# Performance work log

Measured on AMD Instinct MI355X. Metric: run time of the kernel, lower is better.

The kernel has to match this reference:

```python
import jax, jax.numpy as jnp
import numpy as np

T, B, E, H, V, L = 128, 64, 1024, 1024, 10000, 2  # emb_size must equal hidden_size (see decode layer)


def setup_inputs() -> dict:
    key = jax.random.key(0)
    ks = jax.random.split(key, 8)
    s = 0.05
    return {
        "inputs": jax.random.randint(ks[0], (T, B), 0, V),
        "hidden": jnp.zeros((L, B, H), jnp.float32),
        "emb_table": jax.random.normal(ks[1], (V, E), jnp.float32) * s,
        "Ww": jax.random.normal(ks[2], (L, H, E), jnp.float32) * s,
        "Wb": jnp.zeros((L, H), jnp.float32),
        "Uw": jax.random.normal(ks[3], (L, H, H), jnp.float32) * s,
        "Ub": jnp.zeros((L, H), jnp.float32),
        "Fw": jax.random.normal(ks[4], (L, E, H), jnp.float32) * s,
        "Fb": jnp.zeros((L, E), jnp.float32),
        "Dw": jax.random.normal(ks[5], (V, H), jnp.float32) * s,
        "Db": jnp.zeros((V,), jnp.float32),
    }


def reference(inputs, hidden, emb_table, Ww, Wb, Uw, Ub, Fw, Fb, Dw, Db):
    # Dropout is treated as identity (eval mode) for a deterministic reference.
    emb = emb_table[inputs]                     # [T,B,E]

    # --- timestep 0: true recurrence from the provided initial hidden state ---
    x = emb[0]                                  # [B,E]
    h0 = []
    for l in range(L):
        h = jnp.tanh(x @ Ww[l].T + Wb[l] + hidden[l] @ Uw[l].T + Ub[l])  # [B,H]
        x = jnp.tanh(h @ Fw[l].T + Fb[l])                                # [B,E]
        h0.append(h)
    logits0 = x @ Dw.T + Db                     # [B,V]

    # --- timesteps 1..T-1: faithful to the source's indexing bug, the recurrent
    # input h_previous_ts[l] is ALWAYS the timestep-0 state, so all remaining
    # timesteps are independent and can be batched over time. ---
    x = emb[1:]                                 # [T-1,B,E]
    h_rest = []
    for l in range(L):
        aU = h0[l] @ Uw[l].T + Ub[l]            # [B,H], shared across t>=1
        h = jnp.tanh(jnp.einsum('tbe,he->tbh', x, Ww[l]) + Wb[l] + aU)   # [T-1,B,H]
        x = jnp.tanh(jnp.einsum('tbh,eh->tbe', h, Fw[l]) + Fb[l])        # [T-1,B,E]
        h_rest.append(h)
    logits_rest = jnp.einsum('tbe,ve->tbv', x, Dw) + Db  # [T-1,B,V]

    logits = jnp.concatenate([logits0[None], logits_rest], axis=0)        # [T,B,V]

    # Hidden-state list returned by source: [t0_l0, t0_l1, t1_l0, t1_l1, ...]
    h_all = jnp.concatenate(
        [jnp.stack(h0)[None],                               # [1,L,B,H]
         jnp.stack(h_rest).transpose(1, 0, 2, 3)], axis=0   # [T-1,L,B,H]
    ).reshape(T * L, B, H)
    return logits, h_all
```

## Files before the change

kernel.cpp:

```cpp
#include <hip/hip_runtime.h>
#include <hip/hip_bf16.h>
#include <cstdint>
#include <cstddef>

#define T_DIM 128
#define B_DIM 64
#define E_DIM 1024
#define H_DIM 1024
#define V_DIM 10000
#define L_DIM 2
#define VP2   10240
#define MROWS 8192
#define WN    2097152
#define WL    1048576

typedef __bf16 bf16_t;
typedef bf16_t bf16x8 __attribute__((ext_vector_type(8)));
typedef bf16_t bf16x4 __attribute__((ext_vector_type(4)));
typedef float  f32x4  __attribute__((ext_vector_type(4)));

__device__ __forceinline__ void g2l16(const void* g, void* l) {
  __builtin_amdgcn_global_load_lds((const __attribute__((address_space(1))) void*)g,
                                   (__attribute__((address_space(3))) void*)l,
                                   16, 0, 0);
}

__device__ __forceinline__ float fast_tanh(float v) {
  v = fminf(15.f, fmaxf(-15.f, v));
  float e = __expf(2.f * v);
  return (e - 1.f) / (e + 1.f);
}

__global__ __launch_bounds__(512, 2)
void gemm256_bt(const bf16_t* __restrict__ A, const bf16_t* __restrict__ Bm, int K,
                const float* __restrict__ bias, int Nvalid,
                float* __restrict__ outf, long stride_t, int stride_b, int BNT)
{
  constexpr int ASZ = 256 * 64;
  constexpr int BUF = 2 * ASZ;
  __shared__ alignas(16) char lds[4 * BUF];

  const int tid  = threadIdx.x;
  const int wid  = tid >> 6;
  const int lane = tid & 63;
  const int wr = wid >> 2;
  const int wc = wid & 3;
  const int fr = lane & 15;
  const int fq16 = lane >> 4;

  int g   = blockIdx.x;
  int SM  = (gridDim.x / BNT) >> 3;
  int xcd = g & 7;
  int q   = g >> 3;
  int bm  = xcd * SM + (q % SM);
  int bn  = q / SM;

  const bf16_t* gsrc[4];
  int loff[4];
#pragma unroll
  for (int u = 0; u < 4; ++u) {
    int c   = u * 512 + tid;
    int isB = c >> 10;
    int cm  = c & 1023;
    int rp  = cm >> 3, y = cm & 7;
    int u3  = y ^ ((rp & 3) << 1);
    int r0  = (u3 >> 2) & 1;
    int row = rp * 2 + r0;
    int col16 = (u3 & 3) ^ r0;
    const bf16_t* base = isB ? (Bm + (size_t)(bn * 256 + row) * K)
                             : (A  + (size_t)(bm * 256 + row) * K);
    gsrc[u] = base + col16 * 8;
    loff[u] = c * 16;
  }

  int aoff[8], boff[4];
#pragma unroll
  for (int i = 0; i < 8; ++i) {
    int row = wr * 128 + i * 16 + fr;
    int y   = (((row & 1) << 2) | fq16) ^ (row & 7);
    aoff[i] = (row >> 1) * 128 + y * 16;
  }
#pragma unroll
  for (int i = 0; i < 4; ++i) {
    int row = wc * 64 + i * 16 + fr;
    int y   = (((row & 1) << 2) | fq16) ^ (row & 7);
    boff[i] = ASZ + (row >> 1) * 128 + y * 16;
  }

  f32x4 zero = {0.f, 0.f, 0.f, 0.f};
  f32x4 acc[8][4];
#pragma unroll
  for (int i = 0; i < 8; ++i)
#pragma unroll
    for (int j = 0; j < 4; ++j) acc[i][j] = zero;

  const int NT = K >> 5;

#pragma unroll
  for (int u = 0; u < 4; ++u) g2l16(gsrc[u],      lds + 0 * BUF + loff[u]);
#pragma unroll
  for (int u = 0; u < 4; ++u) g2l16(gsrc[u] + 32, lds + 1 * BUF + loff[u]);
#pragma unroll
  for (int u = 0; u < 4; ++u) g2l16(gsrc[u] + 64, lds + 2 * BUF + loff[u]);

  for (int t = 0; t < NT; ++t) {
    if      (t < NT - 2) asm volatile("s_waitcnt vmcnt(8)" ::: "memory");
    else if (t == NT - 2) asm volatile("s_waitcnt vmcnt(4)" ::: "memory");
    else                  asm volatile("s_waitcnt vmcnt(0)" ::: "memory");
    __builtin_amdgcn_sched_barrier(0);
    __builtin_amdgcn_s_barrier();
    asm volatile("" ::: "memory");
    __builtin_amdgcn_sched_barrier(0);

    char* cbuf = lds + (t & 3) * BUF;
    char* sbuf = lds + ((t + 3) & 3) * BUF;
    const int  k3 = (t + 3) << 5;
    const bool st = (t + 3) < NT;

    bf16x8 bfv[4], af[4];
#pragma unroll
    for (int i = 0; i < 4; ++i) bfv[i] = *(const bf16x8*)(cbuf + boff[i]);
#pragma unroll
    for (int i = 0; i < 4; ++i) af[i]  = *(const bf16x8*)(cbuf + aoff[i]);
    if (st) {
      g2l16(gsrc[0] + k3, sbuf + loff[0]);
      g2l16(gsrc[1] + k3, sbuf + loff[1]);
    }
    asm volatile("s_waitcnt lgkmcnt(0)" ::: "memory");
    __builtin_amdgcn_sched_barrier(0);
    __builtin_amdgcn_s_setprio(1);
#pragma unroll
    for (int mi = 0; mi < 4; ++mi)
#pragma unroll
      for (int ni = 0; ni < 4; ++ni)
        acc[mi][ni] = __builtin_amdgcn_mfma_f32_16x16x32_bf16(af[mi], bfv[ni], acc[mi][ni], 0, 0, 0);
    __builtin_amdgcn_s_setprio(0);

#pragma unroll
    for (int i = 0; i < 4; ++i) af[i] = *(const bf16x8*)(cbuf + aoff[4 + i]);
    if (st) {
      g2l16(gsrc[2] + k3, sbuf + loff[2]);
      g2l16(gsrc[3] + k3, sbuf + loff[3]);
    }
    asm volatile("s_waitcnt lgkmcnt(0)" ::: "memory");
    __builtin_amdgcn_sched_barrier(0);
    __builtin_amdgcn_s_setprio(1);
#pragma unroll
    for (int mi = 0; mi < 4; ++mi)
#pragma unroll
      for (int ni = 0; ni < 4; ++ni)
        acc[4 + mi][ni] = __builtin_amdgcn_mfma_f32_16x16x32_bf16(af[mi], bfv[ni], acc[4 + mi][ni], 0, 0, 0);
    __builtin_amdgcn_s_setprio(0);
  }

  const int rb  = (lane >> 4) * 4;
  const int cb_ = lane & 15;
#pragma unroll
  for (int mi = 0; mi < 8; ++mi) {
#pragma unroll
    for (int ni = 0; ni < 4; ++ni) {
      const int col = bn * 256 + wc * 64 + ni * 16 + cb_;
      if (col < Nvalid) {
        const float bv = bias[col];
#pragma unroll
        for (int r = 0; r < 4; ++r) {
          const int row = bm * 256 + wr * 128 + mi * 16 + rb + r;
          long o = (long)(row >> 6) * stride_t + (long)(row & 63) * stride_b + col;
          outf[o] = acc[mi][ni][r] + bv;
        }
      }
    }
  }
}

template<int BK>
__global__ __launch_bounds__(256)
void gemm_bt(const bf16_t* __restrict__ A, const bf16_t* __restrict__ Bm, int K,
             const float* __restrict__ bias, int Nvalid,
             const float* __restrict__ Z, int do_tanh,
             bf16_t* __restrict__ outb, int outb_stride,
             float* __restrict__ outf, long stride_t, int stride_b, int Mvalid,
             int BNT, long abatch, long bbatch, long biasbatch, long obatch)
{
  __shared__ alignas(16) bf16_t lA[128 * BK];
  __shared__ alignas(16) bf16_t lB[128 * BK];
  const int tid  = threadIdx.x;
  const int wid  = tid >> 6;
  const int lane = tid & 63;

  int bm, bn;
  if (BNT > 0) {
    int g   = blockIdx.x;
    int SM  = (gridDim.x / BNT) >> 3;
    int xcd = g & 7;
    int q   = g >> 3;
    bm = xcd * SM + (q % SM);
    bn = q / SM;
  } else {
    bn = blockIdx.x;
    bm = 0;
    int batch = blockIdx.y;
    A    += (size_t)batch * abatch;
    Bm   += (size_t)batch * bbatch;
    bias += (size_t)batch * biasbatch;
    if (outf) outf += (size_t)batch * obatch;
  }

  f32x4 zero = {0.f, 0.f, 0.f, 0.f};
  f32x4 acc[4][4];
#pragma unroll
  for (int i = 0; i < 4; ++i)
#pragma unroll
    for (int j = 0; j < 4; ++j) acc[i][j] = zero;

  constexpr int CW    = BK / 8;
  constexpr int CALLS = (128 * BK / 8) / 256;
  const bf16_t* gA[CALLS];
  const bf16_t* gB[CALLS];
  int ldsoff[CALLS];
#pragma unroll
  for (int u = 0; u < CALLS; ++u) {
    int chunk = (u * 4 + wid) * 64 + lane;
    int row = chunk / CW, cc = chunk % CW;
    gA[u] = A  + (size_t)(bm * 128 + row) * K + cc * 8;
    gB[u] = Bm + (size_t)(bn * 128 + row) * K + cc * 8;
    ldsoff[u] = chunk * 16;
  }

  const int mrow = (wid >> 1) * 64;
  const int ncol = (wid & 1) * 64;
  const int fr = lane & 15;
  const int fq = (lane >> 4) * 16;
  char* lAb = (char*)lA;
  char* lBb = (char*)lB;

  for (int k0 = 0; k0 < K; k0 += BK) {
    __syncthreads();
#pragma unroll
    for (int u = 0; u < CALLS; ++u) g2l16(gA[u] + k0, lAb + ldsoff[u]);
#pragma unroll
    for (int u = 0; u < CALLS; ++u) g2l16(gB[u] + k0, lBb + ldsoff[u]);
    __syncthreads();

#pragma unroll
    for (int kk = 0; kk < BK / 32; ++kk) {
      bf16x8 af[4], bfv[4];
#pragma unroll
      for (int t = 0; t < 4; ++t) {
        af[t]  = *(const bf16x8*)(lAb + (mrow + t * 16 + fr) * (2 * BK) + kk * 64 + fq);
        bfv[t] = *(const bf16x8*)(lBb + (ncol + t * 16 + fr) * (2 * BK) + kk * 64 + fq);
      }
#pragma unroll
      for (int tm = 0; tm < 4; ++tm)
#pragma unroll
        for (int tn = 0; tn < 4; ++tn)
          acc[tm][tn] = __builtin_amdgcn_mfma_f32_16x16x32_bf16(af[tm], bfv[tn], acc[tm][tn], 0, 0, 0);
    }
  }

  const int rb = (lane >> 4) * 4;
  const int cb = lane & 15;
#pragma unroll
  for (int tm = 0; tm < 4; ++tm) {
#pragma unroll
    for (int tn = 0; tn < 4; ++tn) {
      const int col = bn * 128 + ncol + tn * 16 + cb;
      const float bv = (col < Nvalid) ? bias[col] : 0.f;
#pragma unroll
      for (int r = 0; r < 4; ++r) {
        const int row = bm * 128 + mrow + tm * 16 + rb + r;
        float v = acc[tm][tn][r] + bv;
        if (Z) {
          int zr = (row < 64) ? row : 64 + (row & 63);
          v += Z[zr * 1024 + col];
        }
        if (do_tanh) v = fast_tanh(v);
        if (outb) outb[(size_t)row * outb_stride + col] = (bf16_t)v;
        if (outf && row < Mvalid && col < Nvalid) {
          long o = (long)(row >> 6) * stride_t + (long)(row & 63) * stride_b + col;
          outf[o] = v;
        }
      }
    }
  }
}

__global__ void k_cvt3(const float* __restrict__ a, const float* __restrict__ b,
                       const float* __restrict__ c, bf16_t* __restrict__ da,
                       bf16_t* __restrict__ db, bf16_t* __restrict__ dc) {
  int i = blockIdx.x * 256 + threadIdx.x;
  int j = i << 2;
  int sel = j >> 21;
  int loc = j & (WN - 1);
  const float* s = (sel == 0) ? a : (sel == 1) ? b : c;
  bf16_t*      d = (sel == 0) ? da : (sel == 1) ? db : dc;
  f32x4 v = *(const f32x4*)(s + loc);
  bf16x4 o;
#pragma unroll
  for (int k = 0; k < 4; ++k) o[k] = (bf16_t)v[k];
  *(bf16x4*)(d + loc) = o;
}

__global__ void k_cvt_dw4(const float* __restrict__ s, bf16_t* __restrict__ d) {
  int i = blockIdx.x * 256 + threadIdx.x;
  int j = i << 2;
  int r = j >> 10, c = j & 1023;
  f32x4 v = {0.f, 0.f, 0.f, 0.f};
  if (r < V_DIM) v = *(const f32x4*)(s + (size_t)r * 1024 + c);
  bf16x4 o;
#pragma unroll
  for (int k = 0; k < 4; ++k) o[k] = (bf16_t)v[k];
  *(bf16x4*)(d + j) = o;
}

__global__ void k_gather4(const int* __restrict__ inp, const float* __restrict__ etab,
                          bf16_t* __restrict__ X) {
  int i = blockIdx.x * 256 + threadIdx.x;
  int j = i << 2;
  int r = j >> 10, e = j & 1023;
  int idx = inp[r];
  f32x4 v = *(const f32x4*)(etab + (size_t)idx * 1024 + e);
  bf16x4 o;
#pragma unroll
  for (int k = 0; k < 4; ++k) o[k] = (bf16_t)v[k];
  *(bf16x4*)(X + j) = o;
}

__global__ void k_cvt_hidden4(const float* __restrict__ hid, bf16_t* __restrict__ d) {
  int i = blockIdx.x * 256 + threadIdx.x;
  int j = i << 2;
  int l = j >> 17, r = (j >> 10) & 127, e = j & 1023;
  f32x4 v = {0.f, 0.f, 0.f, 0.f};
  if (r < B_DIM) v = *(const f32x4*)(hid + (size_t)(l * B_DIM + r) * 1024 + e);
  bf16x4 o;
#pragma unroll
  for (int k = 0; k < 4; ++k) o[k] = (bf16_t)v[k];
  *(bf16x4*)(d + j) = o;
}

extern "C" void kernel_launch(void* const* d_in, const int* in_sizes, int n_in,
                              void* d_out, int out_size, void* d_ws, size_t ws_size,
                              hipStream_t stream) {
  const int*   inp    = (const int*)  d_in[0];
  const float* hidden = (const float*)d_in[1];
  const float* etab   = (const float*)d_in[2];
  const float* Ww     = (const float*)d_in[3];
  const float* Wb     = (const float*)d_in[4];
  const float* Uw     = (const float*)d_in[5];
  const float* Ub     = (const float*)d_in[6];
  const float* Fw     = (const float*)d_in[7];
  const float* Fb     = (const float*)d_in[8];
  const float* Dw     = (const float*)d_in[9];
  const float* Db     = (const float*)d_in[10];
  float* out = (float*)d_out;

  char* p = (char*)d_ws;
  auto carve = [&](size_t n) { char* r = p; p += (n + 255) & ~(size_t)255; return r; };
  bf16_t* Wbf  = (bf16_t*)carve((size_t)WN * 2);
  bf16_t* Ubf  = (bf16_t*)carve((size_t)WN * 2);
  bf16_t* Fbf  = (bf16_t*)carve((size_t)WN * 2);
  bf16_t* Dbf  = (bf16_t*)carve((size_t)VP2 * 1024 * 2);
  bf16_t* Xc   = (bf16_t*)carve((size_t)MROWS * 1024 * 2);
  bf16_t* Hc   = (bf16_t*)carve((size_t)MROWS * 1024 * 2);
  bf16_t* hidb = (bf16_t*)carve((size_t)L_DIM * 128 * 1024 * 2);
  bf16_t* h0b  = (bf16_t*)carve((size_t)128 * 1024 * 2);
  float*  Zbuf = (float*) carve((size_t)2 * 128 * 1024 * 4);
  float*  Z0 = Zbuf, * Z1 = Zbuf + 131072;

  float* hall = out + (size_t)T_DIM * B_DIM * V_DIM;
  const long ST_H = (long)L_DIM * B_DIM * H_DIM;
  const long ST_V = (long)B_DIM * V_DIM;

  k_cvt3       <<<3 * WN / 4 / 256, 256, 0, stream>>>(Ww, Uw, Fw, Wbf, Ubf, Fbf);
  k_cvt_dw4    <<<VP2 * 1024 / 4 / 256, 256, 0, stream>>>(Dw, Dbf);
  k_gather4    <<<MROWS * 1024 / 4 / 256, 256, 0, stream>>>(inp, etab, Xc);
  k_cvt_hidden4<<<L_DIM * 128 * 1024 / 4 / 256, 256, 0, stream>>>(hidden, hidb);

  gemm_bt<64><<<dim3(8, 2), 256, 0, stream>>>(hidb, Ubf, 1024,
      Ub, 1024, nullptr, 0, nullptr, 0,
      Zbuf, 0L, 1024, 64,
      0, (long)128 * 1024, (long)WL, 1024L, 131072L);

  for (int l = 0; l < L_DIM; ++l) {
    float* Zl = l ? Z1 : Z0;
    gemm_bt<64><<<dim3(8, 1), 256, 0, stream>>>(Xc, Wbf + (size_t)l * WL, 1024,
        Wb + l * 1024, 1024, Zl, 1, h0b, 1024,
        nullptr, 0L, 0, 0, 0, 0, 0, 0, 0);
    gemm_bt<64><<<dim3(8, 1), 256, 0, stream>>>(h0b, Ubf + (size_t)l * WL, 1024,
        Ub + l * 1024, 1024, nullptr, 0, nullptr, 0,
        Zl + 64 * 1024, 0L, 1024, 64, 0, 0, 0, 0, 0);
    gemm_bt<32><<<dim3(64 * 8), 256, 0, stream>>>(Xc, Wbf + (size_t)l * WL, 1024,
        Wb + l * 1024, 1024, Zl, 1, Hc, 1024,
        hall + (size_t)l * B_DIM * H_DIM, ST_H, 1024, MROWS,
        8, 0, 0, 0, 0);
    gemm_bt<32><<<dim3(64 * 8), 256, 0, stream>>>(Hc, Fbf + (size_t)l * WL, 1024,
        Fb + l * 1024, 1024, nullptr, 1, Xc, 1024,
        nullptr, 0L, 0, 0, 8, 0, 0, 0, 0);
  }

  gemm256_bt<<<dim3(32 * 40), 512, 0, stream>>>(Xc, Dbf, 1024,
      Db, V_DIM, out, ST_V, V_DIM, 40);

  (void)in_sizes; (void)n_in; (void)out_size; (void)ws_size;
}
```

Measured before the change: 989.5 us.

## Template the 512-thread GEMM on M-tile and use it for layer GEMMs

```diff
diff --git a/kernel.cpp b/kernel.cpp
--- a/kernel.cpp
+++ b/kernel.cpp
@@ -31,13 +31,29 @@
   return (e - 1.f) / (e + 1.f);
 }
 
+template<int N> __device__ __forceinline__ void waitcnt_vm();
+template<> __device__ __forceinline__ void waitcnt_vm<8>() { asm volatile("s_waitcnt vmcnt(8)" ::: "memory"); }
+template<> __device__ __forceinline__ void waitcnt_vm<6>() { asm volatile("s_waitcnt vmcnt(6)" ::: "memory"); }
+template<> __device__ __forceinline__ void waitcnt_vm<4>() { asm volatile("s_waitcnt vmcnt(4)" ::: "memory"); }
+template<> __device__ __forceinline__ void waitcnt_vm<3>() { asm volatile("s_waitcnt vmcnt(3)" ::: "memory"); }
+template<> __device__ __forceinline__ void waitcnt_vm<0>() { asm volatile("s_waitcnt vmcnt(0)" ::: "memory"); }
+
+template<int BM>
 __global__ __launch_bounds__(512, 2)
 void gemm256_bt(const bf16_t* __restrict__ A, const bf16_t* __restrict__ Bm, int K,
                 const float* __restrict__ bias, int Nvalid,
-                float* __restrict__ outf, long stride_t, int stride_b, int BNT)
+                const float* __restrict__ Z, int do_tanh,
+                bf16_t* __restrict__ outb, int outb_stride,
+                float* __restrict__ outf, long stride_t, int stride_b, int Mvalid,
+                int BNT)
 {
-  constexpr int ASZ = 256 * 64;
-  constexpr int BUF = 2 * ASZ;
+  constexpr int ASZ_A = BM * 64;
+  constexpr int ASZ_B = 256 * 64;
+  constexpr int BUF   = ASZ_A + ASZ_B;
+  constexpr int CALLS = (BM + 256) / 128;
+  constexpr int CA    = 2;
+  constexpr int WROWS = BM / 2;
+  constexpr int MI    = WROWS / 16;
   __shared__ alignas(16) char lds[4 * BUF];
 
   const int tid  = threadIdx.x;
@@ -55,28 +71,28 @@
   int bm  = xcd * SM + (q % SM);
   int bn  = q / SM;
 
-  const bf16_t* gsrc[4];
-  int loff[4];
-#pragma unroll
-  for (int u = 0; u < 4; ++u) {
+  const bf16_t* gsrc[CALLS];
+  int loff[CALLS];
+#pragma unroll
+  for (int u = 0; u < CALLS; ++u) {
     int c   = u * 512 + tid;
-    int isB = c >> 10;
-    int cm  = c & 1023;
+    int isB = (c >= BM * 4) ? 1 : 0;
+    int cm  = isB ? (c - BM * 4) : c;
     int rp  = cm >> 3, y = cm & 7;
     int u3  = y ^ ((rp & 3) << 1);
     int r0  = (u3 >> 2) & 1;
     int row = rp * 2 + r0;
     int col16 = (u3 & 3) ^ r0;
     const bf16_t* base = isB ? (Bm + (size_t)(bn * 256 + row) * K)
-                             : (A  + (size_t)(bm * 256 + row) * K);
+                             : (A  + (size_t)(bm * BM  + row) * K);
     gsrc[u] = base + col16 * 8;
     loff[u] = c * 16;
   }
 
-  int aoff[8], boff[4];
-#pragma unroll
-  for (int i = 0; i < 8; ++i) {
-    int row = wr * 128 + i * 16 + fr;
+  int aoff[MI], boff[4];
+#pragma unroll
+  for (int i = 0; i < MI; ++i) {
+    int row = wr * WROWS + i * 16 + fr;
     int y   = (((row & 1) << 2) | fq16) ^ (row & 7);
     aoff[i] = (row >> 1) * 128 + y * 16;
   }
@@ -84,29 +100,29 @@
   for (int i = 0; i < 4; ++i) {
     int row = wc * 64 + i * 16 + fr;
     int y   = (((row & 1) << 2) | fq16) ^ (row & 7);
-    boff[i] = ASZ + (row >> 1) * 128 + y * 16;
+    boff[i] = ASZ_A + (row >> 1) * 128 + y * 16;
   }
 
   f32x4 zero = {0.f, 0.f, 0.f, 0.f};
-  f32x4 acc[8][4];
-#pragma unroll
-  for (int i = 0; i < 8; ++i)
+  f32x4 acc[MI][4];
+#pragma unroll
+  for (int i = 0; i < MI; ++i)
 #pragma unroll
     for (int j = 0; j < 4; ++j) acc[i][j] = zero;
 
   const int NT = K >> 5;
 
 #pragma unroll
-  for (int u = 0; u < 4; ++u) g2l16(gsrc[u],      lds + 0 * BUF + loff[u]);
-#pragma unroll
-  for (int u = 0; u < 4; ++u) g2l16(gsrc[u] + 32, lds + 1 * BUF + loff[u]);
-#pragma unroll
-  for (int u = 0; u < 4; ++u) g2l16(gsrc[u] + 64, lds + 2 * BUF + loff[u]);
+  for (int u = 0; u < CALLS; ++u) g2l16(gsrc[u],      lds + 0 * BUF + loff[u]);
+#pragma unroll
+  for (int u = 0; u < CALLS; ++u) g2l16(gsrc[u] + 32, lds + 1 * BUF + loff[u]);
+#pragma unroll
+  for (int u = 0; u < CALLS; ++u) g2l16(gsrc[u] + 64, lds + 2 * BUF + loff[u]);
 
   for (int t = 0; t < NT; ++t) {
-    if      (t < NT - 2) asm volatile("s_waitcnt vmcnt(8)" ::: "memory");
-    else if (t == NT - 2) asm volatile("s_waitcnt vmcnt(4)" ::: "memory");
-    else                  asm volatile("s_waitcnt vmcnt(0)" ::: "memory");
+    if      (t < NT - 2)  waitcnt_vm<2 * CALLS>();
+    else if (t == NT - 2) waitcnt_vm<CALLS>();
+    else                  waitcnt_vm<0>();
     __builtin_amdgcn_sched_barrier(0);
     __builtin_amdgcn_s_barrier();
     asm volatile("" ::: "memory");
@@ -117,46 +133,46 @@
     const int  k3 = (t + 3) << 5;
     const bool st = (t + 3) < NT;
 
-    bf16x8 bfv[4], af[4];
+    bf16x8 bfv[4], af[MI / 2];
 #pragma unroll
     for (int i = 0; i < 4; ++i) bfv[i] = *(const bf16x8*)(cbuf + boff[i]);
 #pragma unroll
-    for (int i = 0; i < 4; ++i) af[i]  = *(const bf16x8*)(cbuf + aoff[i]);
+    for (int i = 0; i < MI / 2; ++i) af[i] = *(const bf16x8*)(cbuf + aoff[i]);
     if (st) {
-      g2l16(gsrc[0] + k3, sbuf + loff[0]);
-      g2l16(gsrc[1] + k3, sbuf + loff[1]);
+#pragma unroll
+      for (int u = 0; u < CA; ++u) g2l16(gsrc[u] + k3, sbuf + loff[u]);
     }
     asm volatile("s_waitcnt lgkmcnt(0)" ::: "memory");
     __builtin_amdgcn_sched_barrier(0);
     __builtin_amdgcn_s_setprio(1);
 #pragma unroll
-    for (int mi = 0; mi < 4; ++mi)
+    for (int mi = 0; mi < MI / 2; ++mi)
 #pragma unroll
       for (int ni = 0; ni < 4; ++ni)
         acc[mi][ni] = __builtin_amdgcn_mfma_f32_16x16x32_bf16(af[mi], bfv[ni], acc[mi][ni], 0, 0, 0);
     __builtin_amdgcn_s_setprio(0);
 
 #pragma unroll
-    for (int i = 0; i < 4; ++i) af[i] = *(const bf16x8*)(cbuf + aoff[4 + i]);
+    for (int i = 0; i < MI / 2; ++i) af[i] = *(const bf16x8*)(cbuf + aoff[MI / 2 + i]);
     if (st) {
-      g2l16(gsrc[2] + k3, sbuf + loff[2]);
-      g2l16(gsrc[3] + k3, sbuf + loff[3]);
+#pragma unroll
+      for (int u = CA; u < CALLS; ++u) g2l16(gsrc[u] + k3, sbuf + loff[u]);
     }
     asm volatile("s_waitcnt lgkmcnt(0)" ::: "memory");
     __builtin_amdgcn_sched_barrier(0);
     __builtin_amdgcn_s_setprio(1);
 #pragma unroll
-    for (int mi = 0; mi < 4; ++mi)
+    for (int mi = 0; mi < MI / 2; ++mi)
 #pragma unroll
       for (int ni = 0; ni < 4; ++ni)
-        acc[4 + mi][ni] = __builtin_amdgcn_mfma_f32_16x16x32_bf16(af[mi], bfv[ni], acc[4 + mi][ni], 0, 0, 0);
+        acc[MI / 2 + mi][ni] = __builtin_amdgcn_mfma_f32_16x16x32_bf16(af[mi], bfv[ni], acc[MI / 2 + mi][ni], 0, 0, 0);
     __builtin_amdgcn_s_setprio(0);
   }
 
   const int rb  = (lane >> 4) * 4;
   const int cb_ = lane & 15;
 #pragma unroll
-  for (int mi = 0; mi < 8; ++mi) {
+  for (int mi = 0; mi < MI; ++mi) {
 #pragma unroll
     for (int ni = 0; ni < 4; ++ni) {
       const int col = bn * 256 + wc * 64 + ni * 16 + cb_;
@@ -164,9 +180,18 @@
         const float bv = bias[col];
 #pragma unroll
         for (int r = 0; r < 4; ++r) {
-          const int row = bm * 256 + wr * 128 + mi * 16 + rb + r;
-          long o = (long)(row >> 6) * stride_t + (long)(row & 63) * stride_b + col;
-          outf[o] = acc[mi][ni][r] + bv;
+          const int row = bm * BM + wr * WROWS + mi * 16 + rb + r;
+          float v = acc[mi][ni][r] + bv;
+          if (Z) {
+            int zr = (row < 64) ? row : 64 + (row & 63);
+            v += Z[zr * 1024 + col];
+          }
+          if (do_tanh) v = fast_tanh(v);
+          if (outb) outb[(size_t)row * outb_stride + col] = (bf16_t)v;
+          if (outf && row < Mvalid) {
+            long o = (long)(row >> 6) * stride_t + (long)(row & 63) * stride_b + col;
+            outf[o] = v;
+          }
         }
       }
     }
@@ -285,57 +310,54 @@
   }
 }
 
-__global__ void k_cvt3(const float* __restrict__ a, const float* __restrict__ b,
-                       const float* __restrict__ c, bf16_t* __restrict__ da,
-                       bf16_t* __restrict__ db, bf16_t* __restrict__ dc) {
-  int i = blockIdx.x * 256 + threadIdx.x;
-  int j = i << 2;
-  int sel = j >> 21;
-  int loc = j & (WN - 1);
-  const float* s = (sel == 0) ? a : (sel == 1) ? b : c;
-  bf16_t*      d = (sel == 0) ? da : (sel == 1) ? db : dc;
-  f32x4 v = *(const f32x4*)(s + loc);
+#define NB_CVT3 6144
+#define NB_DW   10240
+#define NB_GA   8192
+#define NB_HID  256
+__global__ void k_prep(const float* __restrict__ Ww, const float* __restrict__ Uw,
+                       const float* __restrict__ Fw, bf16_t* __restrict__ Wbf,
+                       bf16_t* __restrict__ Ubf, bf16_t* __restrict__ Fbf,
+                       const float* __restrict__ Dw, bf16_t* __restrict__ Dbf,
+                       const int* __restrict__ inp, const float* __restrict__ etab,
+                       bf16_t* __restrict__ Xc,
+                       const float* __restrict__ hid, bf16_t* __restrict__ hidb) {
+  int b = blockIdx.x;
   bf16x4 o;
-#pragma unroll
-  for (int k = 0; k < 4; ++k) o[k] = (bf16_t)v[k];
-  *(bf16x4*)(d + loc) = o;
-}
-
-__global__ void k_cvt_dw4(const float* __restrict__ s, bf16_t* __restrict__ d) {
-  int i = blockIdx.x * 256 + threadIdx.x;
-  int j = i << 2;
-  int r = j >> 10, c = j & 1023;
-  f32x4 v = {0.f, 0.f, 0.f, 0.f};
-  if (r < V_DIM) v = *(const f32x4*)(s + (size_t)r * 1024 + c);
-  bf16x4 o;
-#pragma unroll
-  for (int k = 0; k < 4; ++k) o[k] = (bf16_t)v[k];
-  *(bf16x4*)(d + j) = o;
-}
-
-__global__ void k_gather4(const int* __restrict__ inp, const float* __restrict__ etab,
-                          bf16_t* __restrict__ X) {
-  int i = blockIdx.x * 256 + threadIdx.x;
-  int j = i << 2;
-  int r = j >> 10, e = j & 1023;
-  int idx = inp[r];
-  f32x4 v = *(const f32x4*)(etab + (size_t)idx * 1024 + e);
-  bf16x4 o;
-#pragma unroll
-  for (int k = 0; k < 4; ++k) o[k] = (bf16_t)v[k];
-  *(bf16x4*)(X + j) = o;
-}
-
-__global__ void k_cvt_hidden4(const float* __restrict__ hid, bf16_t* __restrict__ d) {
-  int i = blockIdx.x * 256 + threadIdx.x;
-  int j = i << 2;
-  int l = j >> 17, r = (j >> 10) & 127, e = j & 1023;
-  f32x4 v = {0.f, 0.f, 0.f, 0.f};
-  if (r < B_DIM) v = *(const f32x4*)(hid + (size_t)(l * B_DIM + r) * 1024 + e);
-  bf16x4 o;
-#pragma unroll
-  for (int k = 0; k < 4; ++k) o[k] = (bf16_t)v[k];
-  *(bf16x4*)(d + j) = o;
+  if (b < NB_CVT3) {
+    int j = (b * 256 + threadIdx.x) << 2;
+    int sel = j >> 21;
+    int loc = j & (WN - 1);
+    const float* s = (sel == 0) ? Ww : (sel == 1) ? Uw : Fw;
+    bf16_t*      d = (sel == 0) ? Wbf : (sel == 1) ? Ubf : Fbf;
+    f32x4 v = *(const f32x4*)(s + loc);
+#pragma unroll
+    for (int k = 0; k < 4; ++k) o[k] = (bf16_t)v[k];
+    *(bf16x4*)(d + loc) = o;
+  } else if (b < NB_CVT3 + NB_DW) {
+    int j = ((b - NB_CVT3) * 256 + threadIdx.x) << 2;
+    int r = j >> 10, c = j & 1023;
+    f32x4 v = {0.f, 0.f, 0.f, 0.f};
+    if (r < V_DIM) v = *(const f32x4*)(Dw + (size_t)r * 1024 + c);
+#pragma unroll
+    for (int k = 0; k < 4; ++k) o[k] = (bf16_t)v[k];
+    *(bf16x4*)(Dbf + j) = o;
+  } else if (b < NB_CVT3 + NB_DW + NB_GA) {
+    int j = ((b - NB_CVT3 - NB_DW) * 256 + threadIdx.x) << 2;
+    int r = j >> 10, e = j & 1023;
+    int idx = inp[r];
+    f32x4 v = *(const f32x4*)(etab + (size_t)idx * 1024 + e);
+#pragma unroll
+    for (int k = 0; k < 4; ++k) o[k] = (bf16_t)v[k];
+    *(bf16x4*)(Xc + j) = o;
+  } else {
+    int j = ((b - NB_CVT3 - NB_DW - NB_GA) * 256 + threadIdx.x) << 2;
+    int l = j >> 17, r = (j >> 10) & 127, e = j & 1023;
+    f32x4 v = {0.f, 0.f, 0.f, 0.f};
+    if (r < B_DIM) v = *(const f32x4*)(hid + (size_t)(l * B_DIM + r) * 1024 + e);
+#pragma unroll
+    for (int k = 0; k < 4; ++k) o[k] = (bf16_t)v[k];
+    *(bf16x4*)(hidb + j) = o;
+  }
 }
 
 extern "C" void kernel_launch(void* const* d_in, const int* in_sizes, int n_in,
@@ -371,10 +393,8 @@
   const long ST_H = (long)L_DIM * B_DIM * H_DIM;
   const long ST_V = (long)B_DIM * V_DIM;
 
-  k_cvt3       <<<3 * WN / 4 / 256, 256, 0, stream>>>(Ww, Uw, Fw, Wbf, Ubf, Fbf);
-  k_cvt_dw4    <<<VP2 * 1024 / 4 / 256, 256, 0, stream>>>(Dw, Dbf);
-  k_gather4    <<<MROWS * 1024 / 4 / 256, 256, 0, stream>>>(inp, etab, Xc);
-  k_cvt_hidden4<<<L_DIM * 128 * 1024 / 4 / 256, 256, 0, stream>>>(hidden, hidb);
+  k_prep<<<NB_CVT3 + NB_DW + NB_GA + NB_HID, 256, 0, stream>>>(
+      Ww, Uw, Fw, Wbf, Ubf, Fbf, Dw, Dbf, inp, etab, Xc, hidden, hidb);
 
   gemm_bt<64><<<dim3(8, 2), 256, 0, stream>>>(hidb, Ubf, 1024,
       Ub, 1024, nullptr, 0, nullptr, 0,
@@ -389,17 +409,17 @@
     gemm_bt<64><<<dim3(8, 1), 256, 0, stream>>>(h0b, Ubf + (size_t)l * WL, 1024,
         Ub + l * 1024, 1024, nullptr, 0, nullptr, 0,
         Zl + 64 * 1024, 0L, 1024, 64, 0, 0, 0, 0, 0);
-    gemm_bt<32><<<dim3(64 * 8), 256, 0, stream>>>(Xc, Wbf + (size_t)l * WL, 1024,
+    gemm256_bt<128><<<dim3(64 * 4), 512, 0, stream>>>(Xc, Wbf + (size_t)l * WL, 1024,
         Wb + l * 1024, 1024, Zl, 1, Hc, 1024,
-        hall + (size_t)l * B_DIM * H_DIM, ST_H, 1024, MROWS,
-        8, 0, 0, 0, 0);
-    gemm_bt<32><<<dim3(64 * 8), 256, 0, stream>>>(Hc, Fbf + (size_t)l * WL, 1024,
+        hall + (size_t)l * B_DIM * H_DIM, ST_H, 1024, MROWS, 4);
+    gemm256_bt<128><<<dim3(64 * 4), 512, 0, stream>>>(Hc, Fbf + (size_t)l * WL, 1024,
         Fb + l * 1024, 1024, nullptr, 1, Xc, 1024,
-        nullptr, 0L, 0, 0, 8, 0, 0, 0, 0);
-  }
-
-  gemm256_bt<<<dim3(32 * 40), 512, 0, stream>>>(Xc, Dbf, 1024,
-      Db, V_DIM, out, ST_V, V_DIM, 40);
+        nullptr, 0L, 0, 0, 4);
+  }
+
+  gemm256_bt<256><<<dim3(32 * 40), 512, 0, stream>>>(Xc, Dbf, 1024,
+      Db, V_DIM, nullptr, 0, nullptr, 0,
+      out, ST_V, V_DIM, MROWS, 40);
 
   (void)in_sizes; (void)n_in; (void)out_size; (void)ws_size;
 }
```

Result: slower. 1.149 ms (+16.1%).
